# Performance work log

Hardware: AMD Instinct MI355X
Metric: run time of the kernel (lower is better)

Reference implementation:

```python
import jax, jax.numpy as jnp
import numpy as np

N_CAM = 6
N_HEADS = 8
N_POINTS = 4
D = 256  # internal d_model of the deformable attention


def _sine_pos(h, w, d=D):
    # DETR PositionEmbeddingSine, normalize=True, channels-last (h, w, d)
    npf = d // 2
    two_pi = 2.0 * np.pi
    y = jnp.arange(1, h + 1, dtype=jnp.float32) / (h + 1e-6) * two_pi
    x = jnp.arange(1, w + 1, dtype=jnp.float32) / (w + 1e-6) * two_pi
    dim_t = (10000.0 ** (2.0 * (jnp.arange(npf) // 2) / npf)).astype(jnp.float32)
    def enc(v):
        p = v[:, None] / dim_t
        return jnp.stack([jnp.sin(p[:, 0::2]), jnp.cos(p[:, 1::2])], axis=-1).reshape(v.shape[0], -1)
    py, px = enc(y), enc(x)
    return jnp.concatenate([
        jnp.broadcast_to(py[:, None, :], (h, w, npf)),
        jnp.broadcast_to(px[None, :, :], (h, w, npf))], axis=-1)


def _layernorm(x, g, b, eps=1e-5):
    mu = jnp.mean(x, -1, keepdims=True)
    var = jnp.mean((x - mu) ** 2, -1, keepdims=True)
    return (x - mu) * jax.lax.rsqrt(var + eps) * g + b


def _bilinear_gather(kv, loc_x, loc_y, H, W):
    # kv: (b, L, heads, H*W, c); loc_*: (b, Lq, heads, L, P) normalized to [0,1]
    # emulates F.grid_sample(mode='bilinear', padding_mode='zeros', align_corners=False)
    b, L, heads, HW, c = kv.shape
    _, Lq, _, _, P = loc_x.shape
    x = loc_x * W - 0.5
    y = loc_y * H - 0.5
    x0 = jnp.floor(x)
    y0 = jnp.floor(y)
    fx = x - x0
    fy = y - y0
    out = jnp.zeros((b, Lq, heads, L, P, c), kv.dtype)
    for dx in (0, 1):
        for dy in (0, 1):
            xi = x0 + dx
            yi = y0 + dy
            valid = (xi >= 0) & (xi < W) & (yi >= 0) & (yi < H)
            wgt = (fx if dx else 1.0 - fx) * (fy if dy else 1.0 - fy) * valid
            idx = (jnp.clip(yi, 0, H - 1) * W + jnp.clip(xi, 0, W - 1)).astype(jnp.int32)
            idx_t = idx.transpose(0, 3, 2, 1, 4).reshape(b, L, heads, Lq * P, 1)
            g = jnp.take_along_axis(kv, idx_t, axis=3)
            g = g.reshape(b, L, heads, Lq, P, c).transpose(0, 3, 2, 1, 4, 5)
            out = out + wgt[..., None] * g
    return out  # (b, Lq, heads, L, P, c)


def reference(x, conv0_w, conv0_b, conv2_w, conv2_b, cam_emb,
              off_w, off_b, val_w, val_b, key_w, key_b, out_w, out_b,
              conv1_w, conv1_b, norm0_g, norm0_b,
              lin1_w, lin1_b, lin2_w, lin2_b, norm2_g, norm2_b):
    bn, dim, H, W = x.shape
    b = bn // N_CAM
    hd = D // N_HEADS
    HW = H * W
    Lq = N_CAM * HW

    x_nhwc = x.transpose(0, 2, 3, 1)                  # (bn, H, W, dim)
    residual = x_nhwc.reshape(b, Lq, dim)             # b (n h w) d

    src = (x_nhwc @ conv0_w.T + conv0_b).reshape(b, N_CAM, H, W, D)  # conv0 1x1

    pos = _sine_pos(H, W)                              # (H, W, 256)
    spc = src + pos[None, None] + cam_emb[None, :, None, None, :]
    # per-level global descriptor: mean over pixels of conv2(src+pos+cam)
    g = jnp.mean((spc @ conv2_w.T + conv2_b).reshape(b, N_CAM, HW, D), axis=2)  # (b, n, 256)

    src_flat = src.reshape(b, Lq, D)
    query = spc.reshape(b, Lq, D)                      # src + cam + pos (flattened)

    value = src_flat @ val_w.T + val_b
    keys = src_flat @ key_w.T + key_b

    # sampling locations: per-query reference point + learned offsets (normalized)
    offsets = (query @ off_w.T + off_b).reshape(b, Lq, N_HEADS, N_CAM, N_POINTS, 2)
    ry, rx = jnp.meshgrid(
        (jnp.arange(H, dtype=jnp.float32) + 0.5) / H,
        (jnp.arange(W, dtype=jnp.float32) + 0.5) / W, indexing='ij')
    ref = jnp.tile(jnp.stack([rx.ravel(), ry.ravel()], -1), (N_CAM, 1))  # (Lq, 2) as (x, y)
    loc = ref[None, :, None, None, None, :] + offsets / jnp.array([W, H], jnp.float32)

    # gather keys and values in a single bilinear pass (concat on channel)
    kv = jnp.concatenate([
        keys.reshape(b, N_CAM, HW, N_HEADS, hd),
        value.reshape(b, N_CAM, HW, N_HEADS, hd)], axis=-1).transpose(0, 1, 3, 2, 4)
    sampled = _bilinear_gather(kv, loc[..., 0], loc[..., 1], H, W)  # (b,Lq,heads,L,P,2hd)
    k_s, v_s = sampled[..., :hd], sampled[..., hd:]

    # append per-level global token as an extra key/value point per level
    g_h = g.reshape(b, 1, N_CAM, N_HEADS, hd).transpose(0, 1, 3, 2, 4)[:, :, :, :, None, :]
    g_h = jnp.broadcast_to(g_h, (b, Lq, N_HEADS, N_CAM, 1, hd))
    k_all = jnp.concatenate([k_s, g_h], axis=4)        # (b,Lq,heads,L,P+1,hd)
    v_all = jnp.concatenate([v_s, g_h], axis=4)

    # key-aware attention: softmax over all (level, point) sampled keys
    q_h = query.reshape(b, Lq, N_HEADS, hd)
    logits = jnp.einsum('bqhd,bqhlpd->bqhlp', q_h, k_all) / jnp.sqrt(jnp.float32(hd))
    attn = jax.nn.softmax(logits.reshape(b, Lq, N_HEADS, -1), axis=-1).reshape(logits.shape)
    attn_out = jnp.einsum('bqhlp,bqhlpd->bqhd', attn, v_all).reshape(b, Lq, D)
    attn_out = attn_out @ out_w.T + out_b

    out = attn_out @ conv1_w.T + conv1_b               # conv1 1x1 back to dim
    out = _layernorm(residual + out, norm0_g, norm0_b)
    ffn = jax.nn.relu(out @ lin1_w.T + lin1_b) @ lin2_w.T + lin2_b
    out = _layernorm(out + ffn, norm2_g, norm2_b)

    return out.reshape(b, N_CAM, H, W, dim).transpose(0, 1, 4, 2, 3).reshape(bn, dim, H, W)


def setup_inputs() -> dict:
    key = jax.random.key(0)
    ks = jax.random.split(key, 16)
    B, DIM, H, W = 1, 256, 20, 40

    def w(k, shape, s=0.02):
        return jax.random.normal(k, shape, jnp.float32) * s

    n_off = N_HEADS * N_CAM * N_POINTS * 2
    return {
        "x": jax.random.normal(ks[0], (B * N_CAM, DIM, H, W), jnp.float32),
        "conv0_w": w(ks[1], (D, DIM)), "conv0_b": jnp.zeros((D,), jnp.float32),
        "conv2_w": w(ks[2], (D, D)), "conv2_b": jnp.zeros((D,), jnp.float32),
        "cam_emb": jax.random.uniform(ks[3], (N_CAM, D), jnp.float32),
        "off_w": w(ks[4], (n_off, D)),
        "off_b": jax.random.normal(ks[5], (n_off,), jnp.float32) * 0.5,
        "val_w": w(ks[6], (D, D)), "val_b": jnp.zeros((D,), jnp.float32),
        "key_w": w(ks[7], (D, D)), "key_b": jnp.zeros((D,), jnp.float32),
        "out_w": w(ks[8], (D, D)), "out_b": jnp.zeros((D,), jnp.float32),
        "conv1_w": w(ks[9], (DIM, D)), "conv1_b": jnp.zeros((DIM,), jnp.float32),
        "norm0_g": jnp.ones((DIM,), jnp.float32), "norm0_b": jnp.zeros((DIM,), jnp.float32),
        "lin1_w": w(ks[10], (DIM, DIM)), "lin1_b": jnp.zeros((DIM,), jnp.float32),
        "lin2_w": w(ks[11], (DIM, DIM)), "lin2_b": jnp.zeros((DIM,), jnp.float32),
        "norm2_g": jnp.ones((DIM,), jnp.float32), "norm2_b": jnp.zeros((DIM,), jnp.float32),
    }
```

## Files before the change

kernel.cpp:

```cpp
#include <hip/hip_runtime.h>
#include <math.h>

typedef unsigned short u16;
typedef unsigned int u32;

#define NCAM 6
#define NHEADS 8
#define NPOINTS 4
#define DD 256
#define HH 20
#define WW 40
#define HWSZ 800
#define LQ 4800
#define HDIM 32

typedef __attribute__((ext_vector_type(8))) short bf16x8;
typedef __attribute__((ext_vector_type(4))) float f32x4;

__device__ __forceinline__ u16 f2b(float x) {
    union { float f; u32 u; } v;
    v.f = x;
    u32 r = (v.u + 0x7FFFu + ((v.u >> 16) & 1u)) >> 16;
    return (u16)r;
}
__device__ __forceinline__ float lo2f(u32 u) {
    union { u32 u; float f; } v; v.u = u << 16; return v.f;
}
__device__ __forceinline__ float hi2f(u32 u) {
    union { u32 u; float f; } v; v.u = u & 0xFFFF0000u; return v.f;
}
__device__ __forceinline__ float red16(float s) {
    s += __shfl_xor(s, 1);
    s += __shfl_xor(s, 2);
    s += __shfl_xor(s, 4);
    s += __shfl_xor(s, 8);
    return s;
}
__device__ __forceinline__ void gl_lds16(const void* g, void* l) {
    __builtin_amdgcn_global_load_lds(
        (const __attribute__((address_space(1))) void*)g,
        (__attribute__((address_space(3))) void*)l, 16, 0, 0);
}


#define P1_BLOCKS 3362
__global__ __launch_bounds__(256) void prep(
    const float* __restrict__ x, const float* __restrict__ conv0_w,
    const float* __restrict__ conv0_b, const float* __restrict__ key_w,
    const float* __restrict__ key_b, const float* __restrict__ val_w,
    const float* __restrict__ val_b, const float* __restrict__ off_w,
    const float* __restrict__ off_b, const float* __restrict__ lin1_w,
    const float* __restrict__ lin2_w, const float* __restrict__ conv1_w,
    const float* __restrict__ conv1_b, const float* __restrict__ out_w,
    const float* __restrict__ out_b, const float* __restrict__ cam_emb,
    float* __restrict__ pos, u16* __restrict__ xtb_t, float* __restrict__ mu_x,
    u16* __restrict__ Wcat_t, float* __restrict__ bias_cat,
    u16* __restrict__ lin1b_t, u16* __restrict__ lin2b_t,
    u16* __restrict__ wcombb_t, float* __restrict__ bcomb,
    float* __restrict__ camoff, float* __restrict__ posy,
    float* __restrict__ posx) {
    __shared__ float sbuf[1088];
    __shared__ __align__(16) u16 As2[1024];
    __shared__ __align__(16) u16 Bs2[4096];
    int b = blockIdx.x, t = threadIdx.x;
    if (b < 800) {
        int hw = b, d = t;
        int h = hw / WW, w = hw % WW;
        int j = (d & 127) >> 1;
        float dim = powf(10000.0f, (float)j * (1.0f / 64.0f));
        float v;
        if (d < 128) v = (float)(h + 1) / (20.0f + 1e-6f) * (2.0f * (float)M_PI);
        else         v = (float)(w + 1) / (40.0f + 1e-6f) * (2.0f * (float)M_PI);
        float p = v / dim;
        pos[hw * DD + d] = (d & 1) ? cosf(p) : sinf(p);
    } else if (b < 1184) {
        int row = (b - 800) * 4 + (t >> 6);
        int lane = t & 63;
        const float* base = x + (size_t)row * HWSZ;
        float s = 0.f;
        for (int i = lane; i < HWSZ; i += 64) s += base[i];
#pragma unroll
        for (int m = 1; m <= 32; m <<= 1) s += __shfl_xor(s, m);
        if (lane == 0) mu_x[row] = s * (1.0f / (float)HWSZ);
    } else if (b < 1952) {
        int i = (b - 1184) * 256 + t;
        if (i < 65536) {
            int n = i >> 8, k = i & 255;
            Wcat_t[(((size_t)(k >> 3)) * 1152 + n) * 8 + (k & 7)] = f2b(conv0_w[i]);
            if (i < 256) bias_cat[i] = conv0_b[i];
        } else if (i < 131072) {
            int j = i - 65536;
            int n = j >> 8, k = j & 255;
            lin1b_t[(((size_t)(k >> 3)) * 256 + n) * 8 + (k & 7)] = f2b(lin1_w[j]);
        } else {
            int j = i - 131072;
            int n = j >> 8, k = j & 255;
            lin2b_t[(((size_t)(k >> 3)) * 256 + n) * 8 + (k & 7)] = f2b(lin2_w[j]);
        }
    } else if (b < 3152) {
        int idx = b - 1952;
        int cam = idx / 200, rem = idx % 200;
        int hw0 = (rem % 25) * 32, c0 = (rem / 25) * 32;
        float (*tile)[33] = (float(*)[33])sbuf;
        int lhw = t & 31, lc4 = t >> 5;
#pragma unroll
        for (int i = 0; i < 4; ++i) {
            int lc = lc4 * 4 + i;
            tile[lc][lhw] = x[((size_t)(cam * DD + c0 + lc)) * HWSZ + hw0 + lhw];
        }
        __syncthreads();
        int lc2 = t & 31, lhw4 = t >> 5;
        int c = c0 + lc2;
#pragma unroll
        for (int i = 0; i < 4; ++i) {
            int lhw2 = lhw4 * 4 + i;
            int row = cam * HWSZ + hw0 + lhw2;
            xtb_t[(((size_t)(c >> 3)) * 4800 + row) * 8 + (c & 7)] =
                f2b(tile[lc2][lhw2]);
        }
    } else if (b < 3212) {
        int idx = b - 3152;
        int yside = (idx < 20);
        int coord = yside ? idx : idx - 20;
        if (t < 128) {
            int d = t, j = d >> 1;
            float dim = powf(10000.0f, (float)j * (1.0f / 64.0f));
            float v = yside
                ? (float)(coord + 1) / (20.0f + 1e-6f) * (2.0f * (float)M_PI)
                : (float)(coord + 1) / (40.0f + 1e-6f) * (2.0f * (float)M_PI);
            float p = v / dim;
            sbuf[d] = (d & 1) ? cosf(p) : sinf(p);
        }
        __syncthreads();
        int koff = yside ? 0 : 128;
        float* outp = yside ? (posy + coord * 384) : (posx + coord * 384);
        int l = t & 15, og = t >> 4;
#pragma unroll
        for (int chunk = 0; chunk < 24; ++chunk) {
            int n = chunk * 16 + og;
            const float* wr = off_w + (size_t)n * 256 + koff + l * 8;
            float4 w0 = *(const float4*)wr;
            float4 w1 = *(const float4*)(wr + 4);
            const float* pv = sbuf + l * 8;
            float s = pv[0] * w0.x + pv[1] * w0.y + pv[2] * w0.z + pv[3] * w0.w +
                      pv[4] * w1.x + pv[5] * w1.y + pv[6] * w1.z + pv[7] * w1.w;
            s = red16(s);
            if (l == 0) outp[n] = s;
        }
    } else if (b < 3218) {
        int cam = b - 3212;
        sbuf[t] = cam_emb[cam * DD + t];
        __syncthreads();
        int l = t & 15, og = t >> 4;
#pragma unroll
        for (int chunk = 0; chunk < 24; ++chunk) {
            int n = chunk * 16 + og;
            const float* wr = off_w + (size_t)n * 256 + l * 16;
            float s = 0.f;
#pragma unroll
            for (int i = 0; i < 4; ++i) {
                float4 w4 = *(const float4*)(wr + i * 4);
                const float* ce = sbuf + l * 16 + i * 4;
                s += ce[0] * w4.x + ce[1] * w4.y + ce[2] * w4.z + ce[3] * w4.w;
            }
            s = red16(s);
            if (l == 0) camoff[cam * 384 + n] = s;
        }
    } else if (b < 3274) {
        sbuf[t] = conv0_b[t];
        __syncthreads();
        int l = t & 15, og = t >> 4;
        int rr = (b - 3218) * 16 + og;
        const float* srcp;
        float bsrc;
        if (rr < 512) {
            int head = rr >> 6, cpair = (rr >> 1) & 31, kv = rr & 1;
            srcp = (kv ? val_w : key_w) + (size_t)(head * 32 + cpair) * 256;
            bsrc = (kv ? val_b : key_b)[head * 32 + cpair];
        } else {
            srcp = off_w + (size_t)(rr - 512) * 256;
            bsrc = off_b[rr - 512];
        }
        float s = 0.f;
#pragma unroll
        for (int i = 0; i < 4; ++i) {
            float4 w4 = *(const float4*)(srcp + l * 16 + i * 4);
            const float* cb = sbuf + l * 16 + i * 4;
            s += cb[0] * w4.x + cb[1] * w4.y + cb[2] * w4.z + cb[3] * w4.w;
        }
        s = red16(s);
        if (l == 0) bias_cat[256 + rr] = bsrc + s;
    } else if (b < 3290) {
        sbuf[t] = out_b[t];
        __syncthreads();
        int l = t & 15, og = t >> 4;
        int n = (b - 3274) * 16 + og;
        float s = 0.f;
#pragma unroll
        for (int i = 0; i < 4; ++i) {
            float4 w4 = *(const float4*)(conv1_w + (size_t)n * 256 + l * 16 + i * 4);
            const float* ob = sbuf + l * 16 + i * 4;
            s += ob[0] * w4.x + ob[1] * w4.y + ob[2] * w4.z + ob[3] * w4.w;
        }
        s = red16(s);
        if (l == 0) bcomb[n] = conv1_b[n] + s;
    } else {
        int fb = b - 3290;
        int isw = (fb >= 56);
        int bb = isw ? fb - 56 : fb;
        int row0 = (bb >> 1) * 32, col0 = (bb & 1) * 128;
        int wv = t >> 6, lane = t & 63, quad = lane >> 4, l = lane & 15;
        f32x4 acc[2][2] = {};
        for (int k0 = 0; k0 < 256; k0 += 32) {
            __syncthreads();
            if (t < 128) {
                int m = t >> 2, j = t & 3;
                int rr = row0 + m;
                const float* ap;
                if (!isw) {
                    if (rr < 512) {
                        int head = rr >> 6, cpair = (rr >> 1) & 31, kv = rr & 1;
                        ap = (kv ? val_w : key_w) + (size_t)(head * 32 + cpair) * 256;
                    } else {
                        ap = off_w + (size_t)(rr - 512) * 256;
                    }
                } else {
                    ap = conv1_w + (size_t)rr * 256;
                }
                float4 f0 = *(const float4*)&ap[k0 + j * 8];
                float4 f1 = *(const float4*)&ap[k0 + j * 8 + 4];
                uint4 up;
                up.x = (u32)f2b(f0.x) | ((u32)f2b(f0.y) << 16);
                up.y = (u32)f2b(f0.z) | ((u32)f2b(f0.w) << 16);
                up.z = (u32)f2b(f1.x) | ((u32)f2b(f1.y) << 16);
                up.w = (u32)f2b(f1.z) | ((u32)f2b(f1.w) << 16);
                *(uint4*)&As2[(j * 32 + m) * 8] = up;
            }
            {
                int krel = t >> 3;
                int k = k0 + krel;
                int j = t >> 6, kin = k & 7;
                int c0l = (t & 7) * 16;
                const float* wsrc = (isw ? out_w : conv0_w) + (size_t)k * 256 + col0 + c0l;
#pragma unroll
                for (int i = 0; i < 16; i += 4) {
                    float4 f = *(const float4*)&wsrc[i];
                    Bs2[(j * 128 + c0l + i) * 8 + kin]     = f2b(f.x);
                    Bs2[(j * 128 + c0l + i + 1) * 8 + kin] = f2b(f.y);
                    Bs2[(j * 128 + c0l + i + 2) * 8 + kin] = f2b(f.z);
                    Bs2[(j * 128 + c0l + i + 3) * 8 + kin] = f2b(f.w);
                }
            }
            __syncthreads();
            bf16x8 a0 = *(const bf16x8*)&As2[(quad * 32 + l) * 8];
            bf16x8 a1 = *(const bf16x8*)&As2[(quad * 32 + 16 + l) * 8];
            bf16x8 b0v = *(const bf16x8*)&Bs2[(quad * 128 + wv * 32 + l) * 8];
            bf16x8 b1v = *(const bf16x8*)&Bs2[(quad * 128 + wv * 32 + 16 + l) * 8];
            acc[0][0] = __builtin_amdgcn_mfma_f32_16x16x32_bf16(a0, b0v, acc[0][0], 0, 0, 0);
            acc[0][1] = __builtin_amdgcn_mfma_f32_16x16x32_bf16(a0, b1v, acc[0][1], 0, 0, 0);
            acc[1][0] = __builtin_amdgcn_mfma_f32_16x16x32_bf16(a1, b0v, acc[1][0], 0, 0, 0);
            acc[1][1] = __builtin_amdgcn_mfma_f32_16x16x32_bf16(a1, b1v, acc[1][1], 0, 0, 0);
        }
#pragma unroll
        for (int mt = 0; mt < 2; ++mt) {
#pragma unroll
            for (int nt = 0; nt < 2; ++nt) {
                int c = col0 + wv * 32 + nt * 16 + l;
#pragma unroll
                for (int r = 0; r < 4; ++r) {
                    int rr = row0 + mt * 16 + quad * 4 + r;
                    u16 ov = f2b(acc[mt][nt][r]);
                    if (!isw)
                        Wcat_t[(((size_t)(c >> 3)) * 1152 + 256 + rr) * 8 + (c & 7)] = ov;
                    else
                        wcombb_t[(((size_t)(c >> 3)) * 256 + rr) * 8 + (c & 7)] = ov;
                }
            }
        }
    }
}

__global__ __launch_bounds__(256) void gemm_fused(
    const u16* __restrict__ Abt, const u16* __restrict__ Wcat_t,
    const float* __restrict__ bias_cat, const float* __restrict__ pos,
    const float* __restrict__ cam_emb, u16* __restrict__ spcb,
    u16* __restrict__ kvcat16, float* __restrict__ offs,
    const float* __restrict__ mu_x, const float* __restrict__ conv0_w,
    const float* __restrict__ conv0_b, const float* __restrict__ conv2_w,
    const float* __restrict__ conv2_b, float* __restrict__ g) {
    int b = blockIdx.x, t = threadIdx.x;
    if (b < 675) {
        __shared__ __align__(16) u16 As[2048];
        __shared__ __align__(16) u16 Bs[4096];
        int col0 = (b % 9) * 128, row0 = (b / 9) * 64;
        int wv = t >> 6, lane = t & 63;
        int quad = lane >> 4, l = lane & 15;
        f32x4 acc[4][2] = {};
        for (int kg = 0; kg < 32; kg += 4) {
            __syncthreads();
            gl_lds16(Abt + (((size_t)(kg + wv)) * 4800 + row0 + lane) * 8,
                     &As[wv * 64 * 8]);
            int jb = wv >> 1, hb = wv & 1;
            gl_lds16(Wcat_t + (((size_t)(kg + jb)) * 1152 + col0 + hb * 64 + lane) * 8,
                     &Bs[(jb * 128 + hb * 64) * 8]);
            gl_lds16(Wcat_t + (((size_t)(kg + 2 + jb)) * 1152 + col0 + hb * 64 + lane) * 8,
                     &Bs[((2 + jb) * 128 + hb * 64) * 8]);
            __syncthreads();
            bf16x8 b0 = *(const bf16x8*)&Bs[(quad * 128 + wv * 32 + l) * 8];
            bf16x8 b1 = *(const bf16x8*)&Bs[(quad * 128 + wv * 32 + 16 + l) * 8];
#pragma unroll
            for (int mt = 0; mt < 4; ++mt) {
                bf16x8 a = *(const bf16x8*)&As[(quad * 64 + mt * 16 + l) * 8];
                acc[mt][0] = __builtin_amdgcn_mfma_f32_16x16x32_bf16(a, b0, acc[mt][0], 0, 0, 0);
                acc[mt][1] = __builtin_amdgcn_mfma_f32_16x16x32_bf16(a, b1, acc[mt][1], 0, 0, 0);
            }
        }
#pragma unroll
        for (int mt = 0; mt < 4; ++mt) {
#pragma unroll
            for (int nt = 0; nt < 2; ++nt) {
                int col = col0 + wv * 32 + nt * 16 + l;
                float bb = bias_cat[col];
#pragma unroll
                for (int r = 0; r < 4; ++r) {
                    int row = row0 + mt * 16 + quad * 4 + r;
                    float v = acc[mt][nt][r] + bb;
                    if (col0 < 256) {
                        int cam = row / HWSZ, hw = row % HWSZ;
                        spcb[(size_t)row * 256 + col] =
                            f2b(v + pos[(size_t)hw * 256 + col] + cam_emb[cam * 256 + col]);
                    } else if (col0 < 768) {
                        kvcat16[(size_t)row * 512 + (col - 256)] = f2b(v);
                    } else {
                        offs[(size_t)row * 384 + (col - 768)] = v;
                    }
                }
            }
        }
    } else {
        int cam = b - 675;
        __shared__ float mu[DD];
        __shared__ float smu[DD];
        float pm;
        {
            int d = t;
            int j = (d & 127) >> 1;
            float inv = 1.0f / powf(10000.0f, (float)j * (1.0f / 64.0f));
            float s = 0.f;
            if (d < 128) {
                for (int h = 0; h < HH; ++h) {
                    float p = (float)(h + 1) / (20.0f + 1e-6f) * (2.0f * (float)M_PI) * inv;
                    s += (d & 1) ? cosf(p) : sinf(p);
                }
                pm = s * (1.0f / (float)HH);
            } else {
                for (int w = 0; w < WW; ++w) {
                    float p = (float)(w + 1) / (40.0f + 1e-6f) * (2.0f * (float)M_PI) * inv;
                    s += (d & 1) ? cosf(p) : sinf(p);
                }
                pm = s * (1.0f / (float)WW);
            }
        }
        mu[t] = mu_x[cam * DD + t];
        __syncthreads();
        float a = conv0_b[t] + pm + cam_emb[cam * DD + t];
        const float* wr = conv0_w + (size_t)t * DD;
        for (int k = 0; k < DD; ++k) a += mu[k] * wr[k];
        smu[t] = a;
        __syncthreads();
        float ga = conv2_b[t];
        const float* w2r = conv2_w + (size_t)t * DD;
        for (int d = 0; d < DD; ++d) ga += smu[d] * w2r[d];
        g[cam * DD + t] = ga;
    }
}

__global__ __launch_bounds__(256, 4) void attn_kernel(
    const u16* __restrict__ spcb, const u16* __restrict__ kvcat16,
    const float* __restrict__ offs, const float* __restrict__ posy,
    const float* __restrict__ posx, const float* __restrict__ camoff,
    const float* __restrict__ g, u16* __restrict__ attn_out) {
    int qq = blockIdx.x;
    int q0 = qq * 2;
    int tid = threadIdx.x;
    int cam = q0 / HWSZ;
    int hw0 = q0 % HWSZ;
    __shared__ float soff[2][384];
    __shared__ float wgt[2][192][4];
    __shared__ int   idxp[2][192][4];
    for (int i = tid; i < 768; i += 256) {
        int qi = i / 384, n = i - qi * 384;
        int hw = hw0 + qi;
        int h = hw / WW, w = hw - h * WW;
        soff[qi][n] = offs[(size_t)(q0 + qi) * 384 + n] + posy[h * 384 + n] +
                      posx[w * 384 + n] + camoff[cam * 384 + n];
    }
    __syncthreads();
    for (int e2 = tid; e2 < 384; e2 += 256) {
        int qi = e2 / 192, e = e2 - qi * 192;
        int head = e / 24, r = e - head * 24;
        int scam = r >> 2;
        int hw = hw0 + qi;
        int h = hw / WW, w = hw - h * WW;
        float X = (float)w + soff[qi][e * 2];
        float Y = (float)h + soff[qi][e * 2 + 1];
        float x0f = floorf(X), y0f = floorf(Y);
        float fx = X - x0f, fy = Y - y0f;
        int x0 = (int)x0f, y0 = (int)y0f, x1 = x0 + 1, y1 = y0 + 1;
        float vx0 = (x0 >= 0 && x0 < WW) ? 1.f : 0.f;
        float vx1 = (x1 >= 0 && x1 < WW) ? 1.f : 0.f;
        float vy0 = (y0 >= 0 && y0 < HH) ? 1.f : 0.f;
        float vy1 = (y1 >= 0 && y1 < HH) ? 1.f : 0.f;
        int cx0 = min(max(x0, 0), WW - 1), cx1 = min(max(x1, 0), WW - 1);
        int cy0 = min(max(y0, 0), HH - 1), cy1 = min(max(y1, 0), HH - 1);
        wgt[qi][e][0] = (1.f - fx) * (1.f - fy) * vx0 * vy0;
        wgt[qi][e][1] = fx * (1.f - fy) * vx1 * vy0;
        wgt[qi][e][2] = (1.f - fx) * fy * vx0 * vy1;
        wgt[qi][e][3] = fx * fy * vx1 * vy1;
        int pb = scam * HWSZ, hb = head * 64;
        idxp[qi][e][0] = ((pb + cy0 * WW + cx0) << 9) + hb;
        idxp[qi][e][1] = ((pb + cy0 * WW + cx1) << 9) + hb;
        idxp[qi][e][2] = ((pb + cy1 * WW + cx0) << 9) + hb;
        idxp[qi][e][3] = ((pb + cy1 * WW + cx1) << 9) + hb;
    }
    __syncthreads();
    int qi = tid >> 7, head = (tid >> 4) & 7, l = tid & 15;
    int q = q0 + qi;
    int c0 = l * 2;
    u32 qu = *(const u32*)&spcb[(size_t)q * 256 + head * 32 + c0];
    const float scale = 0.17677669529663687f;
    float q0s = lo2f(qu) * scale, q1s = hi2f(qu) * scale;
    float m = -1e30f, den = 0.f, o0 = 0.f, o1 = 0.f;
    int l4 = 4 * l;
    for (int scp = 0; scp < 3; ++scp) {
        int e0i = head * 24 + scp * 8;
        float av0[8], av1[8], lg[8];
#pragma unroll
        for (int p = 0; p < 8; ++p) {
            int e = e0i + p;
            float ak0 = 0.f, ak1 = 0.f, a0 = 0.f, a1 = 0.f;
#pragma unroll
            for (int j = 0; j < 4; ++j) {
                float wj = wgt[qi][e][j];
                int idx = idxp[qi][e][j] + l4;
                uint2 d = *(const uint2*)&kvcat16[idx];
                ak0 += wj * lo2f(d.x);
                a0  += wj * hi2f(d.x);
                ak1 += wj * lo2f(d.y);
                a1  += wj * hi2f(d.y);
            }
            av0[p] = a0; av1[p] = a1;
            float pl = q0s * ak0 + q1s * ak1;
            lg[p] = red16(pl);
        }
        float2 gva = *(const float2*)&g[(scp * 2) * 256 + head * 32 + c0];
        float2 gvb = *(const float2*)&g[(scp * 2 + 1) * 256 + head * 32 + c0];
        float pga = red16(q0s * gva.x + q1s * gva.y);
        float pgb = red16(q0s * gvb.x + q1s * gvb.y);
        float mc = fmaxf(pga, pgb);
#pragma unroll
        for (int p = 0; p < 8; ++p) mc = fmaxf(mc, lg[p]);
        float mn = fmaxf(m, mc);
        float aa = __expf(m - mn);
        float ee[8];
        float dsum = 0.f, s0 = 0.f, s1 = 0.f;
#pragma unroll
        for (int p = 0; p < 8; ++p) {
            ee[p] = __expf(lg[p] - mn);
            dsum += ee[p];
            s0 += ee[p] * av0[p];
            s1 += ee[p] * av1[p];
        }
        float ea = __expf(pga - mn), eb = __expf(pgb - mn);
        dsum += ea + eb;
        s0 += ea * gva.x + eb * gvb.x;
        s1 += ea * gva.y + eb * gvb.y;
        den = den * aa + dsum;
        o0 = o0 * aa + s0;
        o1 = o1 * aa + s1;
        m = mn;
    }
    float inv = 1.f / den;
    u32 pack = (u32)f2b(o0 * inv) | ((u32)f2b(o1 * inv) << 16);
    *(u32*)&attn_out[(size_t)q * 256 + head * 32 + c0] = pack;
}

__global__ __launch_bounds__(256) void epilogue(
    const u16* __restrict__ Ab, const u16* __restrict__ Wc_t,
    const float* __restrict__ bcomb, const float* __restrict__ x_nchw,
    const float* __restrict__ n0g, const float* __restrict__ n0b,
    const u16* __restrict__ W1_t, const float* __restrict__ b1v,
    const u16* __restrict__ W2_t, const float* __restrict__ b2v,
    const float* __restrict__ n2g, const float* __restrict__ n2b,
    float* __restrict__ out_nchw) {
    __shared__ __align__(16) u16 As[552];
    __shared__ __align__(16) u16 Bs[8192];
    __shared__ __align__(16) u16 A2[4360];
    __shared__ float red[4][4][4][2];
    int t = threadIdx.x;
    int row0 = blockIdx.x * 16;
    int wv = t >> 6, lane = t & 63, quad = lane >> 4, l = lane & 15;
    int cam = row0 / HWSZ;
    int hw0q = row0 % HWSZ + quad * 4;

    f32x4 acc[4] = {};
    for (int kg = 0; kg < 32; kg += 4) {
        __syncthreads();
        if (t < 64) {
            int mm = t >> 2, j = t & 3;
            *(uint4*)&As[(j * 17 + mm) * 8] =
                *(const uint4*)&Ab[(size_t)(row0 + mm) * 256 + kg * 8 + j * 8];
        }
#pragma unroll
        for (int s = 0; s < 4; ++s)
            gl_lds16(Wc_t + (((size_t)(kg + wv)) * 256 + s * 64 + lane) * 8,
                     &Bs[(wv * 256 + s * 64) * 8]);
        __syncthreads();
        bf16x8 a = *(const bf16x8*)&As[(quad * 17 + l) * 8];
#pragma unroll
        for (int nt = 0; nt < 4; ++nt) {
            bf16x8 b = *(const bf16x8*)&Bs[(quad * 256 + wv * 64 + nt * 16 + l) * 8];
            acc[nt] = __builtin_amdgcn_mfma_f32_16x16x32_bf16(a, b, acc[nt], 0, 0, 0);
        }
    }
    float v[4][4];
    int cols[4];
#pragma unroll
    for (int nt = 0; nt < 4; ++nt) {
        int col = wv * 64 + nt * 16 + l;
        cols[nt] = col;
        float bb = bcomb[col];
        float4 rx = *(const float4*)&x_nchw[((size_t)(cam * 256 + col)) * HWSZ + hw0q];
        v[nt][0] = acc[nt][0] + bb + rx.x;
        v[nt][1] = acc[nt][1] + bb + rx.y;
        v[nt][2] = acc[nt][2] + bb + rx.z;
        v[nt][3] = acc[nt][3] + bb + rx.w;
    }
#pragma unroll
    for (int r = 0; r < 4; ++r) {
        float s = v[0][r] + v[1][r] + v[2][r] + v[3][r];
        float sq = v[0][r] * v[0][r] + v[1][r] * v[1][r] +
                   v[2][r] * v[2][r] + v[3][r] * v[3][r];
#pragma unroll
        for (int msk = 1; msk <= 8; msk <<= 1) {
            s += __shfl_xor(s, msk);
            sq += __shfl_xor(sq, msk);
        }
        if (l == 0) { red[wv][quad][r][0] = s; red[wv][quad][r][1] = sq; }
    }
    __syncthreads();
    float o0[4][4];
#pragma unroll
    for (int r = 0; r < 4; ++r) {
        float S = red[0][quad][r][0] + red[1][quad][r][0] +
                  red[2][quad][r][0] + red[3][quad][r][0];
        float Q = red[0][quad][r][1] + red[1][quad][r][1] +
                  red[2][quad][r][1] + red[3][quad][r][1];
        float mean = S * (1.0f / 256.0f);
        float var = Q * (1.0f / 256.0f) - mean * mean;
        float rstd = rsqrtf(var + 1e-5f);
        int row = quad * 4 + r;
#pragma unroll
        for (int nt = 0; nt < 4; ++nt) {
            int col = cols[nt];
            float ov = (v[nt][r] - mean) * rstd * n0g[col] + n0b[col];
            o0[nt][r] = ov;
            A2[((col >> 3) * 17 + row) * 8 + (col & 7)] = f2b(ov);
        }
    }
    f32x4 acc2[4] = {};
    for (int kg = 0; kg < 32; kg += 4) {
        __syncthreads();
#pragma unroll
        for (int s = 0; s < 4; ++s)
            gl_lds16(W1_t + (((size_t)(kg + wv)) * 256 + s * 64 + lane) * 8,
                     &Bs[(wv * 256 + s * 64) * 8]);
        __syncthreads();
        bf16x8 a = *(const bf16x8*)&A2[((kg + quad) * 17 + l) * 8];
#pragma unroll
        for (int nt = 0; nt < 4; ++nt) {
            bf16x8 b = *(const bf16x8*)&Bs[(quad * 256 + wv * 64 + nt * 16 + l) * 8];
            acc2[nt] = __builtin_amdgcn_mfma_f32_16x16x32_bf16(a, b, acc2[nt], 0, 0, 0);
        }
    }
    __syncthreads();
#pragma unroll
    for (int nt = 0; nt < 4; ++nt) {
        int col = cols[nt];
        float bb = b1v[col];
#pragma unroll
        for (int r = 0; r < 4; ++r) {
            int row = quad * 4 + r;
            A2[((col >> 3) * 17 + row) * 8 + (col & 7)] = f2b(fmaxf(acc2[nt][r] + bb, 0.f));
        }
    }
    f32x4 acc3[4] = {};
    for (int kg = 0; kg < 32; kg += 4) {
        __syncthreads();
#pragma unroll
        for (int s = 0; s < 4; ++s)
            gl_lds16(W2_t + (((size_t)(kg + wv)) * 256 + s * 64 + lane) * 8,
                     &Bs[(wv * 256 + s * 64) * 8]);
        __syncthreads();
        bf16x8 a = *(const bf16x8*)&A2[((kg + quad) * 17 + l) * 8];
#pragma unroll
        for (int nt = 0; nt < 4; ++nt) {
            bf16x8 b = *(const bf16x8*)&Bs[(quad * 256 + wv * 64 + nt * 16 + l) * 8];
            acc3[nt] = __builtin_amdgcn_mfma_f32_16x16x32_bf16(a, b, acc3[nt], 0, 0, 0);
        }
    }
    float v2[4][4];
#pragma unroll
    for (int nt = 0; nt < 4; ++nt) {
        float bb = b2v[cols[nt]];
#pragma unroll
        for (int r = 0; r < 4; ++r) v2[nt][r] = acc3[nt][r] + bb + o0[nt][r];
    }
    __syncthreads();
#pragma unroll
    for (int r = 0; r < 4; ++r) {
        float s = v2[0][r] + v2[1][r] + v2[2][r] + v2[3][r];
        float sq = v2[0][r] * v2[0][r] + v2[1][r] * v2[1][r] +
                   v2[2][r] * v2[2][r] + v2[3][r] * v2[3][r];
#pragma unroll
        for (int msk = 1; msk <= 8; msk <<= 1) {
            s += __shfl_xor(s, msk);
            sq += __shfl_xor(sq, msk);
        }
        if (l == 0) { red[wv][quad][r][0] = s; red[wv][quad][r][1] = sq; }
    }
    __syncthreads();
    float mean2[4], rstd2[4];
#pragma unroll
    for (int r = 0; r < 4; ++r) {
        float S = red[0][quad][r][0] + red[1][quad][r][0] +
                  red[2][quad][r][0] + red[3][quad][r][0];
        float Q = red[0][quad][r][1] + red[1][quad][r][1] +
                  red[2][quad][r][1] + red[3][quad][r][1];
        mean2[r] = S * (1.0f / 256.0f);
        float var = Q * (1.0f / 256.0f) - mean2[r] * mean2[r];
        rstd2[r] = rsqrtf(var + 1e-5f);
    }
#pragma unroll
    for (int nt = 0; nt < 4; ++nt) {
        int col = cols[nt];
        float gg = n2g[col], bb = n2b[col];
        float4 ov4;
        ov4.x = (v2[nt][0] - mean2[0]) * rstd2[0] * gg + bb;
        ov4.y = (v2[nt][1] - mean2[1]) * rstd2[1] * gg + bb;
        ov4.z = (v2[nt][2] - mean2[2]) * rstd2[2] * gg + bb;
        ov4.w = (v2[nt][3] - mean2[3]) * rstd2[3] * gg + bb;
        *(float4*)&out_nchw[((size_t)(cam * 256 + col)) * HWSZ + hw0q] = ov4;
    }
}

extern "C" void kernel_launch(void* const* d_in, const int* in_sizes, int n_in,
                              void* d_out, int out_size, void* d_ws, size_t ws_size,
                              hipStream_t stream) {
    const float* x       = (const float*)d_in[0];
    const float* conv0_w = (const float*)d_in[1];
    const float* conv0_b = (const float*)d_in[2];
    const float* conv2_w = (const float*)d_in[3];
    const float* conv2_b = (const float*)d_in[4];
    const float* cam_emb = (const float*)d_in[5];
    const float* off_w   = (const float*)d_in[6];
    const float* off_b   = (const float*)d_in[7];
    const float* val_w   = (const float*)d_in[8];
    const float* val_b   = (const float*)d_in[9];
    const float* key_w   = (const float*)d_in[10];
    const float* key_b   = (const float*)d_in[11];
    const float* out_w   = (const float*)d_in[12];
    const float* out_b   = (const float*)d_in[13];
    const float* conv1_w = (const float*)d_in[14];
    const float* conv1_b = (const float*)d_in[15];
    const float* norm0_g = (const float*)d_in[16];
    const float* norm0_b = (const float*)d_in[17];
    const float* lin1_w  = (const float*)d_in[18];
    const float* lin1_b  = (const float*)d_in[19];
    const float* lin2_w  = (const float*)d_in[20];
    const float* lin2_b  = (const float*)d_in[21];
    const float* norm2_g = (const float*)d_in[22];
    const float* norm2_b = (const float*)d_in[23];

    float* ws = (float*)d_ws;
    float* pos      = ws;
    float* mu_x     = pos + 204800;
    float* g        = mu_x + 1536;
    float* camoff   = g + 1536;
    float* posy     = camoff + 2304;
    float* posx     = posy + 7680;
    float* bias_cat = posx + 15360;
    float* bcomb    = bias_cat + 1152;
    float* offs     = bcomb + 256;
    float* f_xtb    = offs + 1843200;
    float* f_spcb   = f_xtb + 614400;
    float* f_kvcat  = f_spcb + 614400;
    float* f_Wcat   = f_kvcat + 1228800;
    float* f_lin1b  = f_Wcat + 147456;
    float* f_lin2b  = f_lin1b + 32768;
    float* f_wcombb = f_lin2b + 32768;

    u16* xtb_t    = (u16*)f_xtb;
    u16* spcb     = (u16*)f_spcb;
    u16* kvcat16  = (u16*)f_kvcat;
    u16* Wcat_t   = (u16*)f_Wcat;
    u16* lin1b_t  = (u16*)f_lin1b;
    u16* lin2b_t  = (u16*)f_lin2b;
    u16* wcombb_t = (u16*)f_wcombb;
    u16* attn_ob  = xtb_t;

    prep<<<P1_BLOCKS, 256, 0, stream>>>(
        x, conv0_w, conv0_b, key_w, key_b, val_w, val_b, off_w, off_b,
        lin1_w, lin2_w, conv1_w, conv1_b, out_w, out_b, cam_emb,
        pos, xtb_t, mu_x, Wcat_t, bias_cat, lin1b_t, lin2b_t, wcombb_t,
        bcomb, camoff, posy, posx);
    gemm_fused<<<681, 256, 0, stream>>>(xtb_t, Wcat_t, bias_cat, pos, cam_emb,
                                        spcb, kvcat16, offs, mu_x, conv0_w,
                                        conv0_b, conv2_w, conv2_b, g);
    attn_kernel<<<LQ / 2, 256, 0, stream>>>(spcb, kvcat16, offs, posy, posx,
                                            camoff, g, attn_ob);
    epilogue<<<300, 256, 0, stream>>>(attn_ob, wcombb_t, bcomb, x,
                                      norm0_g, norm0_b, lin1b_t, lin1_b,
                                      lin2b_t, lin2_b, norm2_g, norm2_b,
                                      (float*)d_out);
}
```

Measured before the change: 200.8 us.

## Restructure attention kernel to four queries per block with 8-lane heads

```diff
diff --git a/kernel.cpp b/kernel.cpp
--- a/kernel.cpp
+++ b/kernel.cpp
@@ -34,6 +34,12 @@
     s += __shfl_xor(s, 2);
     s += __shfl_xor(s, 4);
     s += __shfl_xor(s, 8);
+    return s;
+}
+__device__ __forceinline__ float red8(float s) {
+    s += __shfl_xor(s, 1);
+    s += __shfl_xor(s, 2);
+    s += __shfl_xor(s, 4);
     return s;
 }
 __device__ __forceinline__ void gl_lds16(const void* g, void* l) {
@@ -375,35 +381,29 @@
     }
 }
 
-__global__ __launch_bounds__(256, 4) void attn_kernel(
+__global__ __launch_bounds__(256, 6) void attn_kernel(
     const u16* __restrict__ spcb, const u16* __restrict__ kvcat16,
     const float* __restrict__ offs, const float* __restrict__ posy,
     const float* __restrict__ posx, const float* __restrict__ camoff,
     const float* __restrict__ g, u16* __restrict__ attn_out) {
-    int qq = blockIdx.x;
-    int q0 = qq * 2;
+    int q0 = blockIdx.x * 4;
     int tid = threadIdx.x;
     int cam = q0 / HWSZ;
-    int hw0 = q0 % HWSZ;
-    __shared__ float soff[2][384];
-    __shared__ float wgt[2][192][4];
-    __shared__ int   idxp[2][192][4];
-    for (int i = tid; i < 768; i += 256) {
-        int qi = i / 384, n = i - qi * 384;
-        int hw = hw0 + qi;
-        int h = hw / WW, w = hw - h * WW;
-        soff[qi][n] = offs[(size_t)(q0 + qi) * 384 + n] + posy[h * 384 + n] +
-                      posx[w * 384 + n] + camoff[cam * 384 + n];
-    }
-    __syncthreads();
-    for (int e2 = tid; e2 < 384; e2 += 256) {
-        int qi = e2 / 192, e = e2 - qi * 192;
+    __shared__ float wgt[3200];
+    __shared__ int   idxp[3200];
+    for (int s = tid; s < 768; s += 256) {
+        int qi = s / 192, e = s - qi * 192;
         int head = e / 24, r = e - head * 24;
         int scam = r >> 2;
-        int hw = hw0 + qi;
+        int hw = q0 % HWSZ + qi;
         int h = hw / WW, w = hw - h * WW;
-        float X = (float)w + soff[qi][e * 2];
-        float Y = (float)h + soff[qi][e * 2 + 1];
+        int n = e * 2;
+        float2 o2 = *(const float2*)&offs[(size_t)(q0 + qi) * 384 + n];
+        float2 py = *(const float2*)&posy[h * 384 + n];
+        float2 px = *(const float2*)&posx[w * 384 + n];
+        float2 co = *(const float2*)&camoff[cam * 384 + n];
+        float X = (float)w + o2.x + py.x + px.x + co.x;
+        float Y = (float)h + o2.y + py.y + px.y + co.y;
         float x0f = floorf(X), y0f = floorf(Y);
         float fx = X - x0f, fy = Y - y0f;
         int x0 = (int)x0f, y0 = (int)y0f, x1 = x0 + 1, y1 = y0 + 1;
@@ -413,76 +413,71 @@
         float vy1 = (y1 >= 0 && y1 < HH) ? 1.f : 0.f;
         int cx0 = min(max(x0, 0), WW - 1), cx1 = min(max(x1, 0), WW - 1);
         int cy0 = min(max(y0, 0), HH - 1), cy1 = min(max(y1, 0), HH - 1);
-        wgt[qi][e][0] = (1.f - fx) * (1.f - fy) * vx0 * vy0;
-        wgt[qi][e][1] = fx * (1.f - fy) * vx1 * vy0;
-        wgt[qi][e][2] = (1.f - fx) * fy * vx0 * vy1;
-        wgt[qi][e][3] = fx * fy * vx1 * vy1;
+        int base = (qi * 8 + head) * 100 + r * 4;
+        wgt[base + 0] = (1.f - fx) * (1.f - fy) * vx0 * vy0;
+        wgt[base + 1] = fx * (1.f - fy) * vx1 * vy0;
+        wgt[base + 2] = (1.f - fx) * fy * vx0 * vy1;
+        wgt[base + 3] = fx * fy * vx1 * vy1;
         int pb = scam * HWSZ, hb = head * 64;
-        idxp[qi][e][0] = ((pb + cy0 * WW + cx0) << 9) + hb;
-        idxp[qi][e][1] = ((pb + cy0 * WW + cx1) << 9) + hb;
-        idxp[qi][e][2] = ((pb + cy1 * WW + cx0) << 9) + hb;
-        idxp[qi][e][3] = ((pb + cy1 * WW + cx1) << 9) + hb;
+        idxp[base + 0] = ((pb + cy0 * WW + cx0) << 9) + hb;
+        idxp[base + 1] = ((pb + cy0 * WW + cx1) << 9) + hb;
+        idxp[base + 2] = ((pb + cy1 * WW + cx0) << 9) + hb;
+        idxp[base + 3] = ((pb + cy1 * WW + cx1) << 9) + hb;
     }
     __syncthreads();
-    int qi = tid >> 7, head = (tid >> 4) & 7, l = tid & 15;
-    int q = q0 + qi;
-    int c0 = l * 2;
-    u32 qu = *(const u32*)&spcb[(size_t)q * 256 + head * 32 + c0];
+    int wv = tid >> 6, lane = tid & 63;
+    int head = lane >> 3, l = lane & 7;
+    int q = q0 + wv;
+    int c0 = l * 4;
+    uint2 qu = *(const uint2*)&spcb[(size_t)q * 256 + head * 32 + c0];
     const float scale = 0.17677669529663687f;
-    float q0s = lo2f(qu) * scale, q1s = hi2f(qu) * scale;
-    float m = -1e30f, den = 0.f, o0 = 0.f, o1 = 0.f;
-    int l4 = 4 * l;
-    for (int scp = 0; scp < 3; ++scp) {
-        int e0i = head * 24 + scp * 8;
-        float av0[8], av1[8], lg[8];
-#pragma unroll
-        for (int p = 0; p < 8; ++p) {
-            int e = e0i + p;
-            float ak0 = 0.f, ak1 = 0.f, a0 = 0.f, a1 = 0.f;
+    float q0s = lo2f(qu.x) * scale, q1s = hi2f(qu.x) * scale;
+    float q2s = lo2f(qu.y) * scale, q3s = hi2f(qu.y) * scale;
+    float m = -1e30f, den = 0.f;
+    float o0 = 0.f, o1 = 0.f, o2 = 0.f, o3 = 0.f;
+    int mbase = (wv * 8 + head) * 100;
+    int l8 = 8 * l;
+    for (int sc = 0; sc < NCAM; ++sc) {
+        float av[4][4], lg[4];
+#pragma unroll
+        for (int p = 0; p < 4; ++p) {
+            int eb = mbase + (sc * 4 + p) * 4;
+            float ak0 = 0.f, ak1 = 0.f, ak2 = 0.f, ak3 = 0.f;
+            float a0 = 0.f, a1 = 0.f, a2 = 0.f, a3 = 0.f;
 #pragma unroll
             for (int j = 0; j < 4; ++j) {
-                float wj = wgt[qi][e][j];
-                int idx = idxp[qi][e][j] + l4;
-                uint2 d = *(const uint2*)&kvcat16[idx];
-                ak0 += wj * lo2f(d.x);
-                a0  += wj * hi2f(d.x);
-                ak1 += wj * lo2f(d.y);
-                a1  += wj * hi2f(d.y);
+                float wj = wgt[eb + j];
+                int idx = idxp[eb + j] + l8;
+                uint4 d = *(const uint4*)&kvcat16[idx];
+                ak0 += wj * lo2f(d.x); a0 += wj * hi2f(d.x);
+                ak1 += wj * lo2f(d.y); a1 += wj * hi2f(d.y);
+                ak2 += wj * lo2f(d.z); a2 += wj * hi2f(d.z);
+                ak3 += wj * lo2f(d.w); a3 += wj * hi2f(d.w);
             }
-            av0[p] = a0; av1[p] = a1;
-            float pl = q0s * ak0 + q1s * ak1;
-            lg[p] = red16(pl);
-        }
-        float2 gva = *(const float2*)&g[(scp * 2) * 256 + head * 32 + c0];
-        float2 gvb = *(const float2*)&g[(scp * 2 + 1) * 256 + head * 32 + c0];
-        float pga = red16(q0s * gva.x + q1s * gva.y);
-        float pgb = red16(q0s * gvb.x + q1s * gvb.y);
-        float mc = fmaxf(pga, pgb);
-#pragma unroll
-        for (int p = 0; p < 8; ++p) mc = fmaxf(mc, lg[p]);
+            av[p][0] = a0; av[p][1] = a1; av[p][2] = a2; av[p][3] = a3;
+            float pl = q0s * ak0 + q1s * ak1 + q2s * ak2 + q3s * ak3;
+            lg[p] = red8(pl);
+        }
+        float4 gv = *(const float4*)&g[sc * 256 + head * 32 + c0];
+        float pg = red8(q0s * gv.x + q1s * gv.y + q2s * gv.z + q3s * gv.w);
+        float mc = fmaxf(fmaxf(fmaxf(lg[0], lg[1]), fmaxf(lg[2], lg[3])), pg);
         float mn = fmaxf(m, mc);
         float aa = __expf(m - mn);
-        float ee[8];
-        float dsum = 0.f, s0 = 0.f, s1 = 0.f;
-#pragma unroll
-        for (int p = 0; p < 8; ++p) {
-            ee[p] = __expf(lg[p] - mn);
-            dsum += ee[p];
-            s0 += ee[p] * av0[p];
-            s1 += ee[p] * av1[p];
-        }
-        float ea = __expf(pga - mn), eb = __expf(pgb - mn);
-        dsum += ea + eb;
-        s0 += ea * gva.x + eb * gvb.x;
-        s1 += ea * gva.y + eb * gvb.y;
-        den = den * aa + dsum;
-        o0 = o0 * aa + s0;
-        o1 = o1 * aa + s1;
+        float e0p = __expf(lg[0] - mn), e1p = __expf(lg[1] - mn);
+        float e2p = __expf(lg[2] - mn), e3p = __expf(lg[3] - mn);
+        float egp = __expf(pg - mn);
+        den = den * aa + (e0p + e1p + e2p + e3p + egp);
+        o0 = o0 * aa + e0p * av[0][0] + e1p * av[1][0] + e2p * av[2][0] + e3p * av[3][0] + egp * gv.x;
+        o1 = o1 * aa + e0p * av[0][1] + e1p * av[1][1] + e2p * av[2][1] + e3p * av[3][1] + egp * gv.y;
+        o2 = o2 * aa + e0p * av[0][2] + e1p * av[1][2] + e2p * av[2][2] + e3p * av[3][2] + egp * gv.z;
+        o3 = o3 * aa + e0p * av[0][3] + e1p * av[1][3] + e2p * av[2][3] + e3p * av[3][3] + egp * gv.w;
         m = mn;
     }
     float inv = 1.f / den;
-    u32 pack = (u32)f2b(o0 * inv) | ((u32)f2b(o1 * inv) << 16);
-    *(u32*)&attn_out[(size_t)q * 256 + head * 32 + c0] = pack;
+    uint2 pack;
+    pack.x = (u32)f2b(o0 * inv) | ((u32)f2b(o1 * inv) << 16);
+    pack.y = (u32)f2b(o2 * inv) | ((u32)f2b(o3 * inv) << 16);
+    *(uint2*)&attn_out[(size_t)q * 256 + head * 32 + c0] = pack;
 }
 
 __global__ __launch_bounds__(256) void epilogue(
@@ -717,7 +712,7 @@
     gemm_fused<<<681, 256, 0, stream>>>(xtb_t, Wcat_t, bias_cat, pos, cam_emb,
                                         spcb, kvcat16, offs, mu_x, conv0_w,
                                         conv0_b, conv2_w, conv2_b, g);
-    attn_kernel<<<LQ / 2, 256, 0, stream>>>(spcb, kvcat16, offs, posy, posx,
+    attn_kernel<<<LQ / 4, 256, 0, stream>>>(spcb, kvcat16, offs, posy, posx,
                                             camoff, g, attn_ob);
     epilogue<<<300, 256, 0, stream>>>(attn_ob, wcombb_t, bcomb, x,
                                       norm0_g, norm0_b, lin1b_t, lin1_b,
```

Result: no change. 203.5 us (+1.4%).
